# Kernel tuning notes

Measured on AMD Instinct MI355X. Metric: run time of the kernel, lower is better.

## Reference

```python
import jax, jax.numpy as jnp
import numpy as np
from jax import lax

NUM_WAVES = 8
EPS_PRESENT = 0.0


def setup_inputs() -> dict:
    key = jax.random.key(0)
    k1, k2, k3, k4 = jax.random.split(key, 4)
    N = 512
    x0 = jax.random.uniform(k1, (N,), dtype=jnp.float32)
    logits = 0.01 * jax.random.normal(k2, (N, N), dtype=jnp.float32)
    T = jax.random.uniform(k3, (N, N, N), dtype=jnp.float32)
    target_idx = jax.random.randint(k4, (1,), 0, N)
    return {"x0": x0, "logits": logits, "T": T, "target_idx": target_idx}


def reference(x0, logits, T, target_idx):
    neg_large = jnp.finfo(logits.dtype).min

    def wave(x, _):
        present_p1 = x > EPS_PRESENT                       # [N]
        present_p2 = present_p1.at[target_idx].set(False)  # [N]
        allowed = present_p1[:, None] & present_p2[None, :]  # [N, N]
        masked_logits = jnp.where(allowed, logits, neg_large)
        probs = jax.nn.softmax(masked_logits, axis=1)
        allowed_count = allowed.sum(axis=1, keepdims=True)
        Qi = jnp.where(allowed_count > 0, probs, jnp.zeros_like(probs))
        offspring = jnp.einsum('a,ab,abk->k', x, Qi, T)    # [N]
        x_new = jnp.maximum(x + offspring, 0.0)
        return x_new, None

    x = jnp.maximum(x0, 0.0)
    x, _ = lax.scan(wave, x, None, length=NUM_WAVES)
    return x
```

## Files before the change

### kernel.cpp

```cpp
#include <hip/hip_runtime.h>
#include <float.h>

#define NN 512
#define TB 16
#define R  (NN / TB)

typedef float f32x4 __attribute__((ext_vector_type(4)));


__device__ __forceinline__ void gbar(int* cnt, int* gen, int nb) {
    __syncthreads();
    if (threadIdx.x == 0) {
        __threadfence();
        int mygen = __hip_atomic_load(gen, __ATOMIC_SEQ_CST, __HIP_MEMORY_SCOPE_AGENT);
        int old   = __hip_atomic_fetch_add(cnt, 1, __ATOMIC_SEQ_CST, __HIP_MEMORY_SCOPE_AGENT);
        if (old == nb - 1) {
            __hip_atomic_store(cnt, 0, __ATOMIC_SEQ_CST, __HIP_MEMORY_SCOPE_AGENT);
            __hip_atomic_fetch_add(gen, 1, __ATOMIC_SEQ_CST, __HIP_MEMORY_SCOPE_AGENT);
        } else {
            while (__hip_atomic_load(gen, __ATOMIC_SEQ_CST, __HIP_MEMORY_SCOPE_AGENT) == mygen)
                __builtin_amdgcn_s_sleep(8);
        }
        __threadfence();
    }
    __syncthreads();
}

__global__ __launch_bounds__(512) void k_qis(const float* __restrict__ x0,
                                             const float* __restrict__ logits,
                                             const float* __restrict__ T,
                                             const int* __restrict__ tgt,
                                             float* __restrict__ W0,
                                             int* __restrict__ bar,
                                             int* __restrict__ flags) {
    const int a = blockIdx.x;
    const int t = threadIdx.x;
    if (a == 0) {
        if (t < 8 * TB) flags[t] = 0;
        if (t == 0) bar[0] = 0;
    }
    const int target = tgt[0];

    __shared__ float qs[NN];
    __shared__ float wsum[8];
    __shared__ f32x4 red4[4][128];

    const int  c = t & 127;
    const int  g = t >> 7;
    const bool row_x = (x0[a] > 0.0f);
    const float* Tp = T + (size_t)a * NN * NN + 4 * c;

    f32x4 buf[8];
    if (row_x) {
#pragma unroll
        for (int u = 0; u < 8; ++u)
            buf[u] = __builtin_nontemporal_load(
                reinterpret_cast<const f32x4*>(Tp + (size_t)(g + 4 * u) * NN));
    }

    const float l = logits[(size_t)a * NN + t];
    const int   p = (x0[t] > 0.0f && t != target) ? 1 : 0;
    const float e = p ? expf(fminf(l, 80.0f)) : 0.0f;
    qs[t] = e;
    __syncthreads();

    f32x4 acc = {0.0f, 0.0f, 0.0f, 0.0f};
    if (row_x) {
        for (int i = 0; i < 128; i += 8) {
            f32x4 nxt[8];
            if (i < 120) {
#pragma unroll
                for (int u = 0; u < 8; ++u)
                    nxt[u] = __builtin_nontemporal_load(
                        reinterpret_cast<const f32x4*>(
                            Tp + (size_t)(g + 4 * (i + 8 + u)) * NN));
            }
#pragma unroll
            for (int u = 0; u < 8; ++u) {
                const float qb = qs[g + 4 * (i + u)];
                acc.x = fmaf(qb, buf[u].x, acc.x);
                acc.y = fmaf(qb, buf[u].y, acc.y);
                acc.z = fmaf(qb, buf[u].z, acc.z);
                acc.w = fmaf(qb, buf[u].w, acc.w);
            }
            if (i < 120) {
#pragma unroll
                for (int u = 0; u < 8; ++u) buf[u] = nxt[u];
            }
        }
    }

    float se = e;
#pragma unroll
    for (int off = 32; off > 0; off >>= 1) se += __shfl_xor(se, off, 64);
    if ((t & 63) == 0) wsum[t >> 6] = se;
    red4[g][c] = acc;
    __syncthreads();
    if (t < 128) {
        float sum = wsum[0];
#pragma unroll
        for (int i2 = 1; i2 < 8; ++i2) sum += wsum[i2];
        const float inv = (row_x && sum > 0.0f) ? (1.0f / sum) : 0.0f;
        const f32x4 r0 = red4[0][t], r1 = red4[1][t], r2 = red4[2][t], r3 = red4[3][t];
        f32x4 o;
        o.x = ((r0.x + r1.x) + (r2.x + r3.x)) * inv;
        o.y = ((r0.y + r1.y) + (r2.y + r3.y)) * inv;
        o.z = ((r0.z + r1.z) + (r2.z + r3.z)) * inv;
        o.w = ((r0.w + r1.w) + (r2.w + r3.w)) * inv;
        if ((a >> 2) == t) o[a & 3] += 1.0f;
        *reinterpret_cast<f32x4*>(W0 + (size_t)a * NN + 4 * t) = o;
    }
}

__global__ __launch_bounds__(512) void k_tail(const float* __restrict__ x0,
                                              const float* __restrict__ logits,
                                              const float* __restrict__ T,
                                              const int* __restrict__ tgt,
                                              float* __restrict__ W0,
                                              float* __restrict__ partial,
                                              int* __restrict__ bar,
                                              int* __restrict__ flags,
                                              float* __restrict__ out,
                                              int force) {
    const int bp = blockIdx.x;
    const int t  = threadIdx.x;
    const int target = tgt[0];

    __shared__ float         xs[NN];
    __shared__ float         Wcol[NN][33];
    __shared__ float         red[16][33];
    __shared__ int           wok[8];
    __shared__ unsigned char msk[NN];
    __shared__ int           chg;
    __shared__ float         redf[NN];
    __shared__ int           redi[NN];
    __shared__ float         qs[NN];

    {
        const float xv = fmaxf(x0[t], 0.0f);
        xs[t]  = xv;
        msk[t] = (xv > 0.0f) ? 1 : 0;
        const int ok = __all(xv > 0.0f);
        if ((t & 63) == 0) wok[t >> 6] = ok;
    }
    __syncthreads();
    int allpos = wok[0];
#pragma unroll
    for (int i2 = 1; i2 < 8; ++i2) allpos &= wok[i2];

    const int j = t & 31, seg = t >> 5;

    if (!force && allpos) {
#pragma unroll
        for (int r = 0; r < NN; r += 16) {
            const int row = r + seg;
            Wcol[row][j] = W0[(size_t)row * NN + 32 * bp + j];
        }
        __syncthreads();

        float* xg = partial;
        for (int w = 0; w < 8; ++w) {
            float pa = 0.0f;
#pragma unroll 8
            for (int i = 0; i < 32; ++i)
                pa = fmaf(xs[32 * seg + i], Wcol[32 * seg + i][j], pa);
            red[seg][j] = pa;
            __syncthreads();
            if (t < 32) {
                float s = red[0][t];
#pragma unroll
                for (int s2 = 1; s2 < 16; ++s2) s += red[s2][t];
                const float xn = fmaxf(s, 0.0f);
                __hip_atomic_store(&xg[w * NN + 32 * bp + t], xn,
                                   __ATOMIC_RELAXED, __HIP_MEMORY_SCOPE_AGENT);
            }
            __syncthreads();
            if (t == 0)
                __hip_atomic_store(&flags[w * TB + bp], 1,
                                   __ATOMIC_RELAXED, __HIP_MEMORY_SCOPE_AGENT);
            if (w == 7 && bp != 0) return;
            if (t < TB)
                while (__hip_atomic_load(&flags[w * TB + t],
                                         __ATOMIC_RELAXED, __HIP_MEMORY_SCOPE_AGENT) == 0)
                    __builtin_amdgcn_s_sleep(1);
            __syncthreads();
            const float xv = __hip_atomic_load(&xg[w * NN + t],
                                               __ATOMIC_RELAXED, __HIP_MEMORY_SCOPE_AGENT);
            if (w == 7) {
                out[t] = xv;
                return;
            }
            xs[t] = xv;
            __syncthreads();
        }
        return;
    }
    __syncthreads();

    const int r0 = bp * R;
    for (int w = 0; w < 8; ++w) {
        float* pbuf = partial + (size_t)(w & 1) * TB * NN;
        float pa = 0.0f;
#pragma unroll
        for (int i = 0; i < R; ++i)
            pa = fmaf(xs[r0 + i], W0[(size_t)(r0 + i) * NN + t], pa);
        pbuf[(size_t)bp * NN + t] = pa;

        gbar(&bar[0], &bar[1], TB);

        if (t == 0) chg = 0;
        float dotp = 0.0f;
#pragma unroll 8
        for (int b = 0; b < TB; ++b)
            dotp += pbuf[(size_t)b * NN + t];
        __syncthreads();
        const float xn = fmaxf(dotp, 0.0f);
        const unsigned char nm = (xn > 0.0f) ? 1 : 0;
        if (nm != msk[t]) atomicOr(&chg, 1);
        xs[t]  = xn;
        msk[t] = nm;
        __syncthreads();
        const bool changed = (chg != 0);

        if (w < 7 && changed) {
            gbar(&bar[0], &bar[1], TB);
            for (int r = 0; r < R; ++r) {
                const int a = r0 + r;
                const float l = logits[(size_t)a * NN + t];
                const int   p = (msk[t] && (t != target)) ? 1 : 0;
                redf[t] = p ? l : -FLT_MAX;
                redi[t] = p;
                __syncthreads();
                for (int s = 256; s > 0; s >>= 1) {
                    if (t < s) { redf[t] = fmaxf(redf[t], redf[t + s]); redi[t] += redi[t + s]; }
                    __syncthreads();
                }
                const float mx  = redf[0];
                const int   cnt = redi[0];
                __syncthreads();
                const float e = p ? expf(l - mx) : 0.0f;
                redf[t] = e;
                __syncthreads();
                for (int s = 256; s > 0; s >>= 1) {
                    if (t < s) redf[t] += redf[t + s];
                    __syncthreads();
                }
                const float inv     = 1.0f / redf[0];
                const bool  rowzero = (!msk[a]) || (cnt == 0);
                qs[t] = rowzero ? 0.0f : e * inv;
                __syncthreads();
                float accr = 0.0f;
                if (!rowzero) {
                    const float* Tp = T + (size_t)a * NN * NN + t;
                    for (int b = 0; b < NN; b += 4) {
#pragma unroll
                        for (int u = 0; u < 4; ++u)
                            accr = fmaf(qs[b + u], Tp[(size_t)(b + u) * NN], accr);
                    }
                }
                W0[(size_t)a * NN + t] = accr + ((a == t) ? 1.0f : 0.0f);
                __syncthreads();
            }
            gbar(&bar[0], &bar[1], TB);
        }
    }

    if (bp == 0) out[t] = xs[t];
}

extern "C" void kernel_launch(void* const* d_in, const int* in_sizes, int n_in,
                              void* d_out, int out_size, void* d_ws, size_t ws_size,
                              hipStream_t stream) {
    const float* x0     = (const float*)d_in[0];
    const float* logits = (const float*)d_in[1];
    const float* T      = (const float*)d_in[2];
    const int*   tgt    = (const int*)d_in[3];
    float* out = (float*)d_out;

    float* W0      = (float*)d_ws;
    float* partial = W0 + (size_t)NN * NN;
    int*   bar     = (int*)(partial + 2 * TB * NN);
    int*   flags   = bar + 2;

    const size_t need = ((size_t)NN * NN + 2 * TB * NN) * 4 + (2 + 8 * TB) * 4;
    const int force = (ws_size >= need) ? 0 : 1;

    k_qis<<<512, 512, 0, stream>>>(x0, logits, T, tgt, W0, bar, flags);
    k_tail<<<TB, 512, 0, stream>>>(x0, logits, T, tgt, W0, partial, bar, flags, out, force);
}
```

Baseline: 97.96 us.

## Poll state values as readiness flags and ping-pong T load buffers

```diff
diff --git a/kernel.cpp b/kernel.cpp
--- a/kernel.cpp
+++ b/kernel.cpp
@@ -31,12 +31,14 @@
                                              const float* __restrict__ T,
                                              const int* __restrict__ tgt,
                                              float* __restrict__ W0,
-                                             int* __restrict__ bar,
-                                             int* __restrict__ flags) {
+                                             float* __restrict__ xg,
+                                             int* __restrict__ bar) {
     const int a = blockIdx.x;
     const int t = threadIdx.x;
     if (a == 0) {
-        if (t < 8 * TB) flags[t] = 0;
+#pragma unroll
+        for (int u = 0; u < 8; ++u)
+            xg[u * NN + t] = 0.0f;
         if (t == 0) bar[0] = 0;
     }
     const int target = tgt[0];
@@ -50,13 +52,14 @@
     const bool row_x = (x0[a] > 0.0f);
     const float* Tp = T + (size_t)a * NN * NN + 4 * c;
 
-    f32x4 buf[8];
-    if (row_x) {
-#pragma unroll
-        for (int u = 0; u < 8; ++u)
-            buf[u] = __builtin_nontemporal_load(
-                reinterpret_cast<const f32x4*>(Tp + (size_t)(g + 4 * u) * NN));
-    }
+#define LOADB(BUF, base)                                                      \
+    _Pragma("unroll")                                                         \
+    for (int u = 0; u < 8; ++u)                                               \
+        BUF[u] = __builtin_nontemporal_load(                                  \
+            reinterpret_cast<const f32x4*>(Tp + (size_t)(g + 4 * ((base) + u)) * NN));
+
+    f32x4 bufA[8], bufB[8];
+    if (row_x) { LOADB(bufA, 0); }
 
     const float l = logits[(size_t)a * NN + t];
     const int   p = (x0[t] > 0.0f && t != target) ? 1 : 0;
@@ -66,29 +69,28 @@
 
     f32x4 acc = {0.0f, 0.0f, 0.0f, 0.0f};
     if (row_x) {
-        for (int i = 0; i < 128; i += 8) {
-            f32x4 nxt[8];
-            if (i < 120) {
-#pragma unroll
-                for (int u = 0; u < 8; ++u)
-                    nxt[u] = __builtin_nontemporal_load(
-                        reinterpret_cast<const f32x4*>(
-                            Tp + (size_t)(g + 4 * (i + 8 + u)) * NN));
-            }
+        for (int i = 0; i < 128; i += 16) {
+            LOADB(bufB, i + 8);
 #pragma unroll
             for (int u = 0; u < 8; ++u) {
                 const float qb = qs[g + 4 * (i + u)];
-                acc.x = fmaf(qb, buf[u].x, acc.x);
-                acc.y = fmaf(qb, buf[u].y, acc.y);
-                acc.z = fmaf(qb, buf[u].z, acc.z);
-                acc.w = fmaf(qb, buf[u].w, acc.w);
-            }
-            if (i < 120) {
-#pragma unroll
-                for (int u = 0; u < 8; ++u) buf[u] = nxt[u];
-            }
-        }
-    }
+                acc.x = fmaf(qb, bufA[u].x, acc.x);
+                acc.y = fmaf(qb, bufA[u].y, acc.y);
+                acc.z = fmaf(qb, bufA[u].z, acc.z);
+                acc.w = fmaf(qb, bufA[u].w, acc.w);
+            }
+            if (i + 16 < 128) { LOADB(bufA, i + 16); }
+#pragma unroll
+            for (int u = 0; u < 8; ++u) {
+                const float qb = qs[g + 4 * (i + 8 + u)];
+                acc.x = fmaf(qb, bufB[u].x, acc.x);
+                acc.y = fmaf(qb, bufB[u].y, acc.y);
+                acc.z = fmaf(qb, bufB[u].z, acc.z);
+                acc.w = fmaf(qb, bufB[u].w, acc.w);
+            }
+        }
+    }
+#undef LOADB
 
     float se = e;
 #pragma unroll
@@ -119,7 +121,6 @@
                                               float* __restrict__ W0,
                                               float* __restrict__ partial,
                                               int* __restrict__ bar,
-                                              int* __restrict__ flags,
                                               float* __restrict__ out,
                                               int force) {
     const int bp = blockIdx.x;
@@ -170,22 +171,14 @@
                 float s = red[0][t];
 #pragma unroll
                 for (int s2 = 1; s2 < 16; ++s2) s += red[s2][t];
-                const float xn = fmaxf(s, 0.0f);
-                __hip_atomic_store(&xg[w * NN + 32 * bp + t], xn,
+                __hip_atomic_store(&xg[w * NN + 32 * bp + t], s,
                                    __ATOMIC_RELAXED, __HIP_MEMORY_SCOPE_AGENT);
             }
-            __syncthreads();
-            if (t == 0)
-                __hip_atomic_store(&flags[w * TB + bp], 1,
-                                   __ATOMIC_RELAXED, __HIP_MEMORY_SCOPE_AGENT);
             if (w == 7 && bp != 0) return;
-            if (t < TB)
-                while (__hip_atomic_load(&flags[w * TB + t],
-                                         __ATOMIC_RELAXED, __HIP_MEMORY_SCOPE_AGENT) == 0)
-                    __builtin_amdgcn_s_sleep(1);
-            __syncthreads();
-            const float xv = __hip_atomic_load(&xg[w * NN + t],
-                                               __ATOMIC_RELAXED, __HIP_MEMORY_SCOPE_AGENT);
+            float xv;
+            while ((xv = __hip_atomic_load(&xg[w * NN + t],
+                                           __ATOMIC_RELAXED, __HIP_MEMORY_SCOPE_AGENT)) == 0.0f)
+                __builtin_amdgcn_s_sleep(1);
             if (w == 7) {
                 out[t] = xv;
                 return;
@@ -280,11 +273,10 @@
     float* W0      = (float*)d_ws;
     float* partial = W0 + (size_t)NN * NN;
     int*   bar     = (int*)(partial + 2 * TB * NN);
-    int*   flags   = bar + 2;
-
-    const size_t need = ((size_t)NN * NN + 2 * TB * NN) * 4 + (2 + 8 * TB) * 4;
+
+    const size_t need = ((size_t)NN * NN + 2 * TB * NN) * 4 + 2 * 4;
     const int force = (ws_size >= need) ? 0 : 1;
 
-    k_qis<<<512, 512, 0, stream>>>(x0, logits, T, tgt, W0, bar, flags);
-    k_tail<<<TB, 512, 0, stream>>>(x0, logits, T, tgt, W0, partial, bar, flags, out, force);
-}
+    k_qis<<<512, 512, 0, stream>>>(x0, logits, T, tgt, W0, partial, bar);
+    k_tail<<<TB, 512, 0, stream>>>(x0, logits, T, tgt, W0, partial, bar, out, force);
+}
```

Result: no change. 96.07 us (-1.9%).
